# Optimization experiments

Hardware: AMD Instinct MI355X
Metric: run time of the kernel (lower is better)

Reference implementation:

```python
import jax, jax.numpy as jnp
import numpy as np

B, S, D, H = 2, 2048, 1024, 16
HD = D // H  # head dim = 64


def setup_inputs() -> dict:
    key = jax.random.key(0)
    ks = jax.random.split(key, 9)
    sc = 1.0 / np.sqrt(D)
    x = jax.random.normal(ks[0], (B, S, D), dtype=jnp.float32)
    # weights stored as (in, out); y = x @ W + b (same math as torch Linear with W.T)
    Wq = jax.random.normal(ks[1], (D, D), dtype=jnp.float32) * sc
    Wk = jax.random.normal(ks[2], (D, D), dtype=jnp.float32) * sc
    Wv = jax.random.normal(ks[3], (D, D), dtype=jnp.float32) * sc
    Wo = jax.random.normal(ks[4], (D, D), dtype=jnp.float32) * sc
    bq = jax.random.normal(ks[5], (D,), dtype=jnp.float32) * 0.01
    bk = jax.random.normal(ks[6], (D,), dtype=jnp.float32) * 0.01
    bv = jax.random.normal(ks[7], (D,), dtype=jnp.float32) * 0.01
    bo = jax.random.normal(ks[8], (D,), dtype=jnp.float32) * 0.01
    return {"x": x, "Wq": Wq, "bq": bq, "Wk": Wk, "bk": bk,
            "Wv": Wv, "bv": bv, "Wo": Wo, "bo": bo}


def reference(x, Wq, bq, Wk, bk, Wv, bv, Wo, bo):
    b, s, d = x.shape
    q = (x @ Wq + bq).reshape(b, s, H, HD)
    k = (x @ Wk + bk).reshape(b, s, H, HD)
    v = (x @ Wv + bv).reshape(b, s, H, HD)
    # [b, h, s, s] scores, scaled by sqrt(head_dim)
    scores = jnp.einsum('bqhd,bkhd->bhqk', q, k) / np.sqrt(HD)
    causal = jnp.triu(jnp.ones((s, s), dtype=bool), k=1)  # True above diagonal
    scores = jnp.where(causal, -jnp.inf, scores)
    w = jax.nn.softmax(scores, axis=-1)  # dropout rate 0 -> identity
    ctx = jnp.einsum('bhqk,bkhd->bqhd', w, v).reshape(b, s, d)
    return ctx @ Wo + bo
```

## Files before the change

kernel.cpp:

```cpp
#include <hip/hip_runtime.h>
#include <math.h>

#define BB 2
#define SS 2048
#define DD 1024
#define HH 16
#define HDIM 64

typedef __bf16 bf16_t;
typedef __attribute__((ext_vector_type(8))) __bf16 bf16x8;
typedef __attribute__((ext_vector_type(4))) __bf16 bf16x4;
typedef __attribute__((ext_vector_type(4))) float f32x4;

__device__ inline bf16_t f2bf(float f) {
    unsigned int x; __builtin_memcpy(&x, &f, 4);
    unsigned int r = (x + 0x7FFFu + ((x >> 16) & 1u)) >> 16;
    unsigned short us = (unsigned short)r;
    bf16_t b; __builtin_memcpy(&b, &us, 2); return b;
}
__device__ inline unsigned int fbits(float f) {
    unsigned int x; __builtin_memcpy(&x, &f, 4); return x;
}
__device__ inline unsigned int pack_bf2(float a, float b) {
    return ((fbits(a) + 0x8000u) >> 16) | ((fbits(b) + 0x8000u) & 0xFFFF0000u);
}
__device__ inline void gload16(const void* g, void* lds_base) {
    __builtin_amdgcn_global_load_lds(
        (const __attribute__((address_space(1))) void*)g,
        (__attribute__((address_space(3))) void*)lds_base, 16, 0, 0);
}

__global__ __launch_bounds__(256)
void prep_kernel(const float* __restrict__ x, bf16_t* __restrict__ xb,
                 const float* __restrict__ W0, const float* __restrict__ W1,
                 const float* __restrict__ W2, const float* __restrict__ W3,
                 bf16x8* __restrict__ P0, bf16x8* __restrict__ P1,
                 bf16x8* __restrict__ P2, bf16x8* __restrict__ P3) {
    const int y = blockIdx.y;
    const int tid = threadIdx.x;
    if (y == 0) {
        const int i = blockIdx.x * 256 + tid;
        const float4 v = reinterpret_cast<const float4*>(x)[i];
        bf16x4 o;
        o.x = f2bf(v.x); o.y = f2bf(v.y); o.z = f2bf(v.z); o.w = f2bf(v.w);
        reinterpret_cast<bf16x4*>(xb)[i] = o;
    } else {
        if (blockIdx.x >= 512) return;
        const float* W = (y == 1) ? W0 : (y == 2) ? W1 : (y == 3) ? W2 : W3;
        bf16x8* Wp = (y == 1) ? P0 : (y == 2) ? P1 : (y == 3) ? P2 : P3;
        const int t = blockIdx.x * 256 + tid;
        const int g = t >> 10, n = t & 1023;
        bf16x8 v;
        #pragma unroll
        for (int j = 0; j < 8; ++j) v[j] = f2bf(W[(size_t)(g * 8 + j) * DD + n]);
        Wp[(size_t)g * DD + n] = v;
    }
}

template<int MODE>
__global__ __launch_bounds__(256)
void gemm_mfma(const bf16_t* __restrict__ A,
               const bf16x8* __restrict__ Wp0, const bf16x8* __restrict__ Wp1,
               const bf16x8* __restrict__ Wp2,
               const float* __restrict__ b0, const float* __restrict__ b1,
               const float* __restrict__ b2,
               void* __restrict__ C0, void* __restrict__ C1,
               bf16_t* __restrict__ Vt) {
    extern __shared__ char smem[];
    bf16x8 (*As)[8]   = reinterpret_cast<bf16x8(*)[8]>(smem);
    bf16x8 (*Bs)[128] = reinterpret_cast<bf16x8(*)[128]>(smem + 16384);

    const int z = (MODE == 0) ? blockIdx.z : 0;
    const bf16x8* Wp = (z == 0) ? Wp0 : (z == 1) ? Wp1 : Wp2;
    const float* bias = (z == 0) ? b0 : (z == 1) ? b1 : b2;

    const int tid = threadIdx.x;
    const int ln = tid & 63, wv = tid >> 6;
    const int quad = ln >> 4, l15 = ln & 15;
    const int wr = wv >> 1, wc = wv & 1;
    const int m0 = blockIdx.y * 128;
    const int n0 = blockIdx.x * 128;

    int arow[4], acl[4], bg[4], bn[4];
    #pragma unroll
    for (int u = 0; u < 4; ++u) {
        const int S = (wv * 4 + u) * 64 + ln;
        arow[u] = S >> 3; acl[u] = (S & 7) ^ (arow[u] & 7);
        bg[u] = S >> 7;   bn[u] = S & 127;
    }

    f32x4 acc[4][4];
    #pragma unroll
    for (int i = 0; i < 4; ++i)
        #pragma unroll
        for (int j = 0; j < 4; ++j) acc[i][j] = (f32x4){0.f, 0.f, 0.f, 0.f};

    for (int k0 = 0; k0 < DD; k0 += 64) {
        __syncthreads();
        const int kg0 = k0 >> 3;
        #pragma unroll
        for (int u = 0; u < 4; ++u) {
            gload16(&A[(size_t)(m0 + arow[u]) * DD + k0 + acl[u] * 8],
                    smem + (size_t)(wv * 4 + u) * 1024);
            gload16(&Wp[(size_t)(kg0 + bg[u]) * DD + n0 + bn[u]],
                    smem + 16384 + (size_t)(wv * 4 + u) * 1024);
        }
        __syncthreads();

        #pragma unroll
        for (int kk = 0; kk < 2; ++kk) {
            bf16x8 fa[4], fb[4];
            #pragma unroll
            for (int mi = 0; mi < 4; ++mi) {
                const int row = wr * 64 + mi * 16 + l15;
                fa[mi] = As[row][(kk * 4 + quad) ^ (row & 7)];
            }
            #pragma unroll
            for (int ni = 0; ni < 4; ++ni)
                fb[ni] = Bs[kk * 4 + quad][wc * 64 + ni * 16 + l15];
            #pragma unroll
            for (int mi = 0; mi < 4; ++mi)
                #pragma unroll
                for (int ni = 0; ni < 4; ++ni)
                    acc[mi][ni] = __builtin_amdgcn_mfma_f32_16x16x32_bf16(
                        fa[mi], fb[ni], acc[mi][ni], 0, 0, 0);
        }
    }

    if (MODE == 1) {
        float* C = (float*)C0;
        #pragma unroll
        for (int ni = 0; ni < 4; ++ni) {
            const int col = n0 + wc * 64 + ni * 16 + l15;
            const float bv = bias[col];
            #pragma unroll
            for (int mi = 0; mi < 4; ++mi)
                #pragma unroll
                for (int r = 0; r < 4; ++r) {
                    const int row = m0 + wr * 64 + mi * 16 + quad * 4 + r;
                    C[(size_t)row * DD + col] = acc[mi][ni][r] + bv;
                }
        }
    } else if (z < 2) {
        bf16_t* C = (bf16_t*)((z == 0) ? C0 : C1);
        #pragma unroll
        for (int ni = 0; ni < 4; ++ni) {
            const int col = n0 + wc * 64 + ni * 16 + l15;
            const float bv = bias[col];
            #pragma unroll
            for (int mi = 0; mi < 4; ++mi)
                #pragma unroll
                for (int r = 0; r < 4; ++r) {
                    const int row = m0 + wr * 64 + mi * 16 + quad * 4 + r;
                    C[(size_t)row * DD + col] = f2bf(acc[mi][ni][r] + bv);
                }
        }
    } else {
        unsigned short (*T)[136] = reinterpret_cast<unsigned short(*)[136]>(smem);
        __syncthreads();
        #pragma unroll
        for (int ni = 0; ni < 4; ++ni) {
            const int cl = wc * 64 + ni * 16 + l15;
            const float bv = bias[n0 + cl];
            #pragma unroll
            for (int mi = 0; mi < 4; ++mi) {
                const int rl = wr * 64 + mi * 16 + quad * 4;
                uint2 pk;
                pk.x = pack_bf2(acc[mi][ni][0] + bv, acc[mi][ni][1] + bv);
                pk.y = pack_bf2(acc[mi][ni][2] + bv, acc[mi][ni][3] + bv);
                *reinterpret_cast<uint2*>(&T[cl][rl]) = pk;
            }
        }
        __syncthreads();
        const int b = m0 >> 11, s0 = m0 & 2047, h0 = n0 >> 6;
        #pragma unroll
        for (int u = 0; u < 8; ++u) {
            const int c = u * 256 + tid;
            const int s8 = c & 15, nl = c >> 4;
            const bf16x8 v = *reinterpret_cast<const bf16x8*>(&T[nl][s8 * 8]);
            const int bh = b * 16 + h0 + (nl >> 6), d = nl & 63;
            *reinterpret_cast<bf16x8*>(
                &Vt[((size_t)bh * 64 + d) * SS + s0 + s8 * 8]) = v;
        }
    }
}

#define SCL 0.18033688f
#define FM  12.0f

__global__ __launch_bounds__(256)
void attn_mfma(const bf16_t* __restrict__ Q, const bf16_t* __restrict__ Kg,
               const bf16_t* __restrict__ Vt, bf16_t* __restrict__ Ctx) {
    __shared__ bf16x8 Ks[128][8];
    __shared__ bf16x8 Vs[128][8];
    __shared__ unsigned short Ps[4][16][64];

    const int tid = threadIdx.x;
    const int ln = tid & 63, w = tid >> 6;
    const int quad = ln >> 4, l15 = ln & 15;
    const int bh = blockIdx.x;
    const int qt = (blockIdx.y + blockIdx.x) & 31;
    const int b = bh >> 4, h = bh & 15;
    const size_t rowbase = (size_t)b * SS;
    const int col0 = h * 64;

    const int krow0 = w * 16 + (ln >> 3);
    const int krow1 = krow0 + 8;
    const int kc0 = (ln & 7) ^ (krow0 & 7);
    const int kc1 = (ln & 7) ^ (krow1 & 7);

    bf16x8 fq[2];
    {
        const int qrow = qt * 64 + w * 16 + l15;
        #pragma unroll
        for (int kk = 0; kk < 2; ++kk)
            fq[kk] = *reinterpret_cast<const bf16x8*>(
                &Q[(rowbase + qrow) * DD + col0 + kk * 32 + quad * 8]);
    }

    f32x4 acc_o[4];
    #pragma unroll
    for (int i = 0; i < 4; ++i) acc_o[i] = (f32x4){0.f, 0.f, 0.f, 0.f};
    float lsum = 0.f;

    auto stage = [&](int tile, int half) {
        char* kb = (char*)&Ks[half * 64][0] + w * 2048;
        char* vb = (char*)&Vs[half * 64][0] + w * 2048;
        gload16(&Kg[(rowbase + tile * 64 + krow0) * DD + col0 + kc0 * 8], kb);
        gload16(&Kg[(rowbase + tile * 64 + krow1) * DD + col0 + kc1 * 8], kb + 1024);
        gload16(&Vt[((size_t)bh * 64 + krow0) * SS + tile * 64 + kc0 * 8], vb);
        gload16(&Vt[((size_t)bh * 64 + krow1) * SS + tile * 64 + kc1 * 8], vb + 1024);
    };

    unsigned short* const psw = &Ps[w][l15][0];
    const int swz = l15 & 7;

    auto compute_tile = [&](int half, bool diag) {
        const int ro = half * 64;
        #pragma unroll
        for (int ni = 0; ni < 4; ++ni) {
            const int slot = ni * 4 + quad;
            unsigned short* pdst =
                psw + (((slot >> 1) ^ swz) * 8 + (slot & 1) * 4);
            if (diag && ni > w) {
                *reinterpret_cast<uint2*>(pdst) = (uint2){0u, 0u};
                continue;
            }
            f32x4 st = (f32x4){0.f, 0.f, 0.f, 0.f};
            const int krow = ni * 16 + l15;
            #pragma unroll
            for (int kk = 0; kk < 2; ++kk) {
                const bf16x8 fk = Ks[ro + krow][(kk * 4 + quad) ^ (krow & 7)];
                st = __builtin_amdgcn_mfma_f32_16x16x32_bf16(fk, fq[kk], st, 0, 0, 0);
            }
            float p[4];
            #pragma unroll
            for (int r = 0; r < 4; ++r) {
                p[r] = __builtin_amdgcn_exp2f(st[r] * SCL - FM);
                if (diag && ni == w && (quad * 4 + r) > l15) p[r] = 0.f;
            }
            lsum += (p[0] + p[1]) + (p[2] + p[3]);
            uint2 pk;
            pk.x = pack_bf2(p[0], p[1]);
            pk.y = pack_bf2(p[2], p[3]);
            *reinterpret_cast<uint2*>(pdst) = pk;
        }
        #pragma unroll
        for (int kk = 0; kk < 2; ++kk) {
            const bf16x8 fp = *reinterpret_cast<const bf16x8*>(
                psw + ((kk * 4 + quad) ^ swz) * 8);
            #pragma unroll
            for (int nd = 0; nd < 4; ++nd) {
                const int vrow = nd * 16 + l15;
                const bf16x8 fv = Vs[ro + vrow][(kk * 4 + quad) ^ (vrow & 7)];
                acc_o[nd] = __builtin_amdgcn_mfma_f32_16x16x32_bf16(fv, fp, acc_o[nd], 0, 0, 0);
            }
        }
    };

    int kt = 0;
    if ((qt & 1) == 0) {
        stage(0, 0);
        __syncthreads();
        compute_tile(0, qt == 0);
        kt = 1;
    }
    for (; kt < qt; kt += 2) {
        __syncthreads();
        stage(kt, 0);
        stage(kt + 1, 1);
        __syncthreads();
        compute_tile(0, false);
        compute_tile(1, kt + 1 == qt);
    }

    lsum += __shfl_xor(lsum, 16);
    lsum += __shfl_xor(lsum, 32);
    const float inv = 1.f / lsum;

    const size_t orow = (rowbase + qt * 64 + w * 16 + l15) * DD + col0;
    #pragma unroll
    for (int nd = 0; nd < 4; ++nd) {
        uint2 ov;
        ov.x = pack_bf2(acc_o[nd][0] * inv, acc_o[nd][1] * inv);
        ov.y = pack_bf2(acc_o[nd][2] * inv, acc_o[nd][3] * inv);
        *reinterpret_cast<uint2*>(&Ctx[orow + nd * 16 + quad * 4]) = ov;
    }
}

extern "C" void kernel_launch(void* const* d_in, const int* in_sizes, int n_in,
                              void* d_out, int out_size, void* d_ws, size_t ws_size,
                              hipStream_t stream) {
    const float* x  = (const float*)d_in[0];
    const float* Wq = (const float*)d_in[1];
    const float* bq = (const float*)d_in[2];
    const float* Wk = (const float*)d_in[3];
    const float* bk = (const float*)d_in[4];
    const float* Wv = (const float*)d_in[5];
    const float* bv = (const float*)d_in[6];
    const float* Wo = (const float*)d_in[7];
    const float* bo = (const float*)d_in[8];
    float* out = (float*)d_out;

    const size_t M = (size_t)BB * SS;
    const size_t mat = M * DD;
    const size_t wsz = (size_t)DD * DD;

    bf16_t* ws = (bf16_t*)d_ws;
    bf16_t* xb   = ws;
    bf16_t* Wqp  = ws + mat;
    bf16_t* Wkp  = Wqp + wsz;
    bf16_t* Wvp  = Wkp + wsz;
    bf16_t* Wop  = Wvp + wsz;
    bf16_t* Qb   = Wop + wsz;
    bf16_t* Kb   = Qb + mat;
    bf16_t* Vtb  = Kb + mat;
    bf16_t* Ctxb = Vtb + mat;

    dim3 blk(256);
    hipLaunchKernelGGL(prep_kernel, dim3(4096, 5), blk, 0, stream,
                       x, xb, Wq, Wk, Wv, Wo,
                       (bf16x8*)Wqp, (bf16x8*)Wkp, (bf16x8*)Wvp, (bf16x8*)Wop);

    hipLaunchKernelGGL((gemm_mfma<0>), dim3(DD / 128, M / 128, 3), blk, 34816, stream,
                       xb, (const bf16x8*)Wqp, (const bf16x8*)Wkp, (const bf16x8*)Wvp,
                       bq, bk, bv, Qb, Kb, Vtb);

    hipLaunchKernelGGL(attn_mfma, dim3(BB * HH, SS / 64), blk, 0, stream,
                       Qb, Kb, Vtb, Ctxb);

    hipLaunchKernelGGL((gemm_mfma<1>), dim3(DD / 128, M / 128, 1), blk, 32768, stream,
                       Ctxb, (const bf16x8*)Wop, (const bf16x8*)Wop, (const bf16x8*)Wop,
                       bo, bo, bo, out, out, nullptr);
}
```

Measured before the change: 199.3 us.

## Enlarge attention query tile, add narrow output GEMM, compact prep grid

Attention now processes 128 query rows per block, two 16-row groups per wave, so each staged K/V tile is reused for twice as many queries, halving K/V loads per query. Query tiles are paired so blocks with short and long causal ranges interleave. The output projection moves to a dedicated kernel with 128x64 tiles, doubling block count for better CU occupancy. The prep kernel drops idle blocks and processes all four weights per thread. More registers per attention wave may reduce occupancy.

```diff
diff --git a/kernel.cpp b/kernel.cpp
--- a/kernel.cpp
+++ b/kernel.cpp
@@ -36,41 +36,45 @@
                  const float* __restrict__ W2, const float* __restrict__ W3,
                  bf16x8* __restrict__ P0, bf16x8* __restrict__ P1,
                  bf16x8* __restrict__ P2, bf16x8* __restrict__ P3) {
-    const int y = blockIdx.y;
-    const int tid = threadIdx.x;
-    if (y == 0) {
-        const int i = blockIdx.x * 256 + tid;
-        const float4 v = reinterpret_cast<const float4*>(x)[i];
-        bf16x4 o;
-        o.x = f2bf(v.x); o.y = f2bf(v.y); o.z = f2bf(v.z); o.w = f2bf(v.w);
-        reinterpret_cast<bf16x4*>(xb)[i] = o;
+    const int bid = blockIdx.x, tid = threadIdx.x;
+    if (bid < 2048) {
+        const int i = bid * 512 + tid;
+        #pragma unroll
+        for (int u = 0; u < 2; ++u) {
+            const int j = i + u * 256;
+            const float4 v = reinterpret_cast<const float4*>(x)[j];
+            bf16x4 o;
+            o.x = f2bf(v.x); o.y = f2bf(v.y); o.z = f2bf(v.z); o.w = f2bf(v.w);
+            reinterpret_cast<bf16x4*>(xb)[j] = o;
+        }
     } else {
-        if (blockIdx.x >= 512) return;
-        const float* W = (y == 1) ? W0 : (y == 2) ? W1 : (y == 3) ? W2 : W3;
-        bf16x8* Wp = (y == 1) ? P0 : (y == 2) ? P1 : (y == 3) ? P2 : P3;
-        const int t = blockIdx.x * 256 + tid;
+        const int t = (bid - 2048) * 256 + tid;
         const int g = t >> 10, n = t & 1023;
-        bf16x8 v;
-        #pragma unroll
-        for (int j = 0; j < 8; ++j) v[j] = f2bf(W[(size_t)(g * 8 + j) * DD + n]);
-        Wp[(size_t)g * DD + n] = v;
-    }
-}
-
-template<int MODE>
+        const float* Ws[4] = {W0, W1, W2, W3};
+        bf16x8* Pp[4] = {P0, P1, P2, P3};
+        #pragma unroll
+        for (int m = 0; m < 4; ++m) {
+            bf16x8 v;
+            #pragma unroll
+            for (int j = 0; j < 8; ++j) v[j] = f2bf(Ws[m][(size_t)(g * 8 + j) * DD + n]);
+            Pp[m][(size_t)g * DD + n] = v;
+        }
+    }
+}
+
 __global__ __launch_bounds__(256)
-void gemm_mfma(const bf16_t* __restrict__ A,
-               const bf16x8* __restrict__ Wp0, const bf16x8* __restrict__ Wp1,
-               const bf16x8* __restrict__ Wp2,
-               const float* __restrict__ b0, const float* __restrict__ b1,
-               const float* __restrict__ b2,
-               void* __restrict__ C0, void* __restrict__ C1,
-               bf16_t* __restrict__ Vt) {
+void gemm_qkv(const bf16_t* __restrict__ A,
+              const bf16x8* __restrict__ Wp0, const bf16x8* __restrict__ Wp1,
+              const bf16x8* __restrict__ Wp2,
+              const float* __restrict__ b0, const float* __restrict__ b1,
+              const float* __restrict__ b2,
+              bf16_t* __restrict__ C0, bf16_t* __restrict__ C1,
+              bf16_t* __restrict__ Vt) {
     extern __shared__ char smem[];
     bf16x8 (*As)[8]   = reinterpret_cast<bf16x8(*)[8]>(smem);
     bf16x8 (*Bs)[128] = reinterpret_cast<bf16x8(*)[128]>(smem + 16384);
 
-    const int z = (MODE == 0) ? blockIdx.z : 0;
+    const int z = blockIdx.z;
     const bf16x8* Wp = (z == 0) ? Wp0 : (z == 1) ? Wp1 : Wp2;
     const float* bias = (z == 0) ? b0 : (z == 1) ? b1 : b2;
 
@@ -127,22 +131,8 @@
         }
     }
 
-    if (MODE == 1) {
-        float* C = (float*)C0;
-        #pragma unroll
-        for (int ni = 0; ni < 4; ++ni) {
-            const int col = n0 + wc * 64 + ni * 16 + l15;
-            const float bv = bias[col];
-            #pragma unroll
-            for (int mi = 0; mi < 4; ++mi)
-                #pragma unroll
-                for (int r = 0; r < 4; ++r) {
-                    const int row = m0 + wr * 64 + mi * 16 + quad * 4 + r;
-                    C[(size_t)row * DD + col] = acc[mi][ni][r] + bv;
-                }
-        }
-    } else if (z < 2) {
-        bf16_t* C = (bf16_t*)((z == 0) ? C0 : C1);
+    if (z < 2) {
+        bf16_t* C = (z == 0) ? C0 : C1;
         #pragma unroll
         for (int ni = 0; ni < 4; ++ni) {
             const int col = n0 + wc * 64 + ni * 16 + l15;
@@ -185,6 +175,84 @@
     }
 }
 
+__global__ __launch_bounds__(256)
+void gemm_out(const bf16_t* __restrict__ A, const bf16x8* __restrict__ Wp,
+              const float* __restrict__ bias, float* __restrict__ C) {
+    __shared__ bf16x8 As[128][8];
+    __shared__ bf16x8 Bs[8][64];
+
+    const int tid = threadIdx.x;
+    const int ln = tid & 63, wv = tid >> 6;
+    const int quad = ln >> 4, l15 = ln & 15;
+    const int wr = wv >> 1, wc = wv & 1;
+    const int m0 = blockIdx.y * 128;
+    const int n0 = blockIdx.x * 64;
+
+    int arow[4], acl[4], bkg[2], bn[2];
+    #pragma unroll
+    for (int u = 0; u < 4; ++u) {
+        const int S = (wv * 4 + u) * 64 + ln;
+        arow[u] = S >> 3; acl[u] = (S & 7) ^ (arow[u] & 7);
+    }
+    #pragma unroll
+    for (int u = 0; u < 2; ++u) {
+        const int S = (wv * 2 + u) * 64 + ln;
+        bkg[u] = S >> 6; bn[u] = S & 63;
+    }
+
+    f32x4 acc[4][2];
+    #pragma unroll
+    for (int i = 0; i < 4; ++i)
+        #pragma unroll
+        for (int j = 0; j < 2; ++j) acc[i][j] = (f32x4){0.f, 0.f, 0.f, 0.f};
+
+    for (int k0 = 0; k0 < DD; k0 += 64) {
+        __syncthreads();
+        const int kg0 = k0 >> 3;
+        #pragma unroll
+        for (int u = 0; u < 4; ++u)
+            gload16(&A[(size_t)(m0 + arow[u]) * DD + k0 + acl[u] * 8],
+                    (char*)&As[0][0] + (size_t)(wv * 4 + u) * 1024);
+        #pragma unroll
+        for (int u = 0; u < 2; ++u)
+            gload16(&Wp[(size_t)(kg0 + bkg[u]) * DD + n0 + bn[u]],
+                    (char*)&Bs[0][0] + (size_t)(wv * 2 + u) * 1024);
+        __syncthreads();
+
+        #pragma unroll
+        for (int kk = 0; kk < 2; ++kk) {
+            bf16x8 fa[4], fb[2];
+            #pragma unroll
+            for (int mi = 0; mi < 4; ++mi) {
+                const int row = wr * 64 + mi * 16 + l15;
+                fa[mi] = As[row][(kk * 4 + quad) ^ (row & 7)];
+            }
+            #pragma unroll
+            for (int ni = 0; ni < 2; ++ni)
+                fb[ni] = Bs[kk * 4 + quad][wc * 32 + ni * 16 + l15];
+            #pragma unroll
+            for (int mi = 0; mi < 4; ++mi)
+                #pragma unroll
+                for (int ni = 0; ni < 2; ++ni)
+                    acc[mi][ni] = __builtin_amdgcn_mfma_f32_16x16x32_bf16(
+                        fa[mi], fb[ni], acc[mi][ni], 0, 0, 0);
+        }
+    }
+
+    #pragma unroll
+    for (int ni = 0; ni < 2; ++ni) {
+        const int col = n0 + wc * 32 + ni * 16 + l15;
+        const float bv = bias[col];
+        #pragma unroll
+        for (int mi = 0; mi < 4; ++mi)
+            #pragma unroll
+            for (int r = 0; r < 4; ++r) {
+                const int row = m0 + wr * 64 + mi * 16 + quad * 4 + r;
+                C[(size_t)row * DD + col] = acc[mi][ni][r] + bv;
+            }
+    }
+}
+
 #define SCL 0.18033688f
 #define FM  12.0f
 
@@ -193,13 +261,14 @@
                const bf16_t* __restrict__ Vt, bf16_t* __restrict__ Ctx) {
     __shared__ bf16x8 Ks[128][8];
     __shared__ bf16x8 Vs[128][8];
-    __shared__ unsigned short Ps[4][16][64];
+    __shared__ unsigned short Ps[4][2][16][64];
 
     const int tid = threadIdx.x;
     const int ln = tid & 63, w = tid >> 6;
     const int quad = ln >> 4, l15 = ln & 15;
     const int bh = blockIdx.x;
-    const int qt = (blockIdx.y + blockIdx.x) & 31;
+    const int tswz = (blockIdx.x + blockIdx.y) & 7;
+    const int qt = (blockIdx.y < 8) ? tswz : 15 - tswz;
     const int b = bh >> 4, h = bh & 15;
     const size_t rowbase = (size_t)b * SS;
     const int col0 = h * 64;
@@ -209,19 +278,22 @@
     const int kc0 = (ln & 7) ^ (krow0 & 7);
     const int kc1 = (ln & 7) ^ (krow1 & 7);
 
-    bf16x8 fq[2];
-    {
-        const int qrow = qt * 64 + w * 16 + l15;
+    bf16x8 fq[2][2];
+    #pragma unroll
+    for (int rg = 0; rg < 2; ++rg) {
+        const int qrow = qt * 128 + w * 32 + rg * 16 + l15;
         #pragma unroll
         for (int kk = 0; kk < 2; ++kk)
-            fq[kk] = *reinterpret_cast<const bf16x8*>(
+            fq[rg][kk] = *reinterpret_cast<const bf16x8*>(
                 &Q[(rowbase + qrow) * DD + col0 + kk * 32 + quad * 8]);
     }
 
-    f32x4 acc_o[4];
-    #pragma unroll
-    for (int i = 0; i < 4; ++i) acc_o[i] = (f32x4){0.f, 0.f, 0.f, 0.f};
-    float lsum = 0.f;
+    f32x4 acc_o[2][4];
+    #pragma unroll
+    for (int rg = 0; rg < 2; ++rg)
+        #pragma unroll
+        for (int i = 0; i < 4; ++i) acc_o[rg][i] = (f32x4){0.f, 0.f, 0.f, 0.f};
+    float lsum[2] = {0.f, 0.f};
 
     auto stage = [&](int tile, int half) {
         char* kb = (char*)&Ks[half * 64][0] + w * 2048;
@@ -232,79 +304,94 @@
         gload16(&Vt[((size_t)bh * 64 + krow1) * SS + tile * 64 + kc1 * 8], vb + 1024);
     };
 
-    unsigned short* const psw = &Ps[w][l15][0];
     const int swz = l15 & 7;
 
-    auto compute_tile = [&](int half, bool diag) {
-        const int ro = half * 64;
-        #pragma unroll
-        for (int ni = 0; ni < 4; ++ni) {
-            const int slot = ni * 4 + quad;
-            unsigned short* pdst =
-                psw + (((slot >> 1) ^ swz) * 8 + (slot & 1) * 4);
-            if (diag && ni > w) {
-                *reinterpret_cast<uint2*>(pdst) = (uint2){0u, 0u};
-                continue;
-            }
-            f32x4 st = (f32x4){0.f, 0.f, 0.f, 0.f};
-            const int krow = ni * 16 + l15;
-            #pragma unroll
-            for (int kk = 0; kk < 2; ++kk) {
-                const bf16x8 fk = Ks[ro + krow][(kk * 4 + quad) ^ (krow & 7)];
-                st = __builtin_amdgcn_mfma_f32_16x16x32_bf16(fk, fq[kk], st, 0, 0, 0);
-            }
-            float p[4];
-            #pragma unroll
-            for (int r = 0; r < 4; ++r) {
-                p[r] = __builtin_amdgcn_exp2f(st[r] * SCL - FM);
-                if (diag && ni == w && (quad * 4 + r) > l15) p[r] = 0.f;
-            }
-            lsum += (p[0] + p[1]) + (p[2] + p[3]);
-            uint2 pk;
-            pk.x = pack_bf2(p[0], p[1]);
-            pk.y = pack_bf2(p[2], p[3]);
-            *reinterpret_cast<uint2*>(pdst) = pk;
+    auto compute_tile = [&](int ro, int dq0, int dq1) {
+        const int dq[2] = {dq0, dq1};
+        #pragma unroll
+        for (int rg = 0; rg < 2; ++rg) {
+            if (dq[rg] < 0) continue;
+            unsigned short* const psw = &Ps[w][rg][l15][0];
+            #pragma unroll
+            for (int ni = 0; ni < 4; ++ni) {
+                const int slot = ni * 4 + quad;
+                unsigned short* pdst = psw + (((slot >> 1) ^ swz) * 8 + (slot & 1) * 4);
+                const int g = ni * 16;
+                if (g > dq[rg]) {
+                    *reinterpret_cast<uint2*>(pdst) = (uint2){0u, 0u};
+                    continue;
+                }
+                f32x4 st = (f32x4){0.f, 0.f, 0.f, 0.f};
+                const int krow = ni * 16 + l15;
+                #pragma unroll
+                for (int kk = 0; kk < 2; ++kk) {
+                    const bf16x8 fk = Ks[ro + krow][(kk * 4 + quad) ^ (krow & 7)];
+                    st = __builtin_amdgcn_mfma_f32_16x16x32_bf16(fk, fq[rg][kk], st, 0, 0, 0);
+                }
+                float p[4];
+                #pragma unroll
+                for (int r = 0; r < 4; ++r) {
+                    p[r] = __builtin_amdgcn_exp2f(st[r] * SCL - FM);
+                    if (g == dq[rg] && (quad * 4 + r) > l15) p[r] = 0.f;
+                }
+                lsum[rg] += (p[0] + p[1]) + (p[2] + p[3]);
+                uint2 pk;
+                pk.x = pack_bf2(p[0], p[1]);
+                pk.y = pack_bf2(p[2], p[3]);
+                *reinterpret_cast<uint2*>(pdst) = pk;
+            }
         }
         #pragma unroll
         for (int kk = 0; kk < 2; ++kk) {
-            const bf16x8 fp = *reinterpret_cast<const bf16x8*>(
-                psw + ((kk * 4 + quad) ^ swz) * 8);
+            bf16x8 fp[2];
+            #pragma unroll
+            for (int rg = 0; rg < 2; ++rg)
+                fp[rg] = *reinterpret_cast<const bf16x8*>(
+                    &Ps[w][rg][l15][(((kk * 4 + quad) ^ swz) * 8)]);
             #pragma unroll
             for (int nd = 0; nd < 4; ++nd) {
                 const int vrow = nd * 16 + l15;
                 const bf16x8 fv = Vs[ro + vrow][(kk * 4 + quad) ^ (vrow & 7)];
-                acc_o[nd] = __builtin_amdgcn_mfma_f32_16x16x32_bf16(fv, fp, acc_o[nd], 0, 0, 0);
+                if (dq0 >= 0)
+                    acc_o[0][nd] = __builtin_amdgcn_mfma_f32_16x16x32_bf16(fv, fp[0], acc_o[0][nd], 0, 0, 0);
+                if (dq1 >= 0)
+                    acc_o[1][nd] = __builtin_amdgcn_mfma_f32_16x16x32_bf16(fv, fp[1], acc_o[1][nd], 0, 0, 0);
             }
         }
     };
 
-    int kt = 0;
-    if ((qt & 1) == 0) {
-        stage(0, 0);
-        __syncthreads();
-        compute_tile(0, qt == 0);
-        kt = 1;
-    }
-    for (; kt < qt; kt += 2) {
-        __syncthreads();
-        stage(kt, 0);
-        stage(kt + 1, 1);
-        __syncthreads();
-        compute_tile(0, false);
-        compute_tile(1, kt + 1 == qt);
-    }
-
-    lsum += __shfl_xor(lsum, 16);
-    lsum += __shfl_xor(lsum, 32);
-    const float inv = 1.f / lsum;
-
-    const size_t orow = (rowbase + qt * 64 + w * 16 + l15) * DD + col0;
-    #pragma unroll
-    for (int nd = 0; nd < 4; ++nd) {
-        uint2 ov;
-        ov.x = pack_bf2(acc_o[nd][0] * inv, acc_o[nd][1] * inv);
-        ov.y = pack_bf2(acc_o[nd][2] * inv, acc_o[nd][3] * inv);
-        *reinterpret_cast<uint2*>(&Ctx[orow + nd * 16 + quad * 4]) = ov;
+    for (int p = 0; p < qt; ++p) {
+        __syncthreads();
+        stage(2 * p, 0);
+        stage(2 * p + 1, 1);
+        __syncthreads();
+        compute_tile(0, 112, 112);
+        compute_tile(64, 112, 112);
+    }
+    {
+        __syncthreads();
+        stage(2 * qt, 0);
+        stage(2 * qt + 1, 1);
+        __syncthreads();
+        const int lq0 = w * 32, lq1 = w * 32 + 16;
+        compute_tile(0, lq0, lq1);
+        compute_tile(64, lq0 - 64, lq1 - 64);
+    }
+
+    #pragma unroll
+    for (int rg = 0; rg < 2; ++rg) {
+        float s = lsum[rg];
+        s += __shfl_xor(s, 16);
+        s += __shfl_xor(s, 32);
+        const float inv = 1.f / s;
+        const size_t orow = (rowbase + qt * 128 + w * 32 + rg * 16 + l15) * DD + col0;
+        #pragma unroll
+        for (int nd = 0; nd < 4; ++nd) {
+            uint2 ov;
+            ov.x = pack_bf2(acc_o[rg][nd][0] * inv, acc_o[rg][nd][1] * inv);
+            ov.y = pack_bf2(acc_o[rg][nd][2] * inv, acc_o[rg][nd][3] * inv);
+            *reinterpret_cast<uint2*>(&Ctx[orow + nd * 16 + quad * 4]) = ov;
+        }
     }
 }
 
@@ -338,18 +425,17 @@
     bf16_t* Ctxb = Vtb + mat;
 
     dim3 blk(256);
-    hipLaunchKernelGGL(prep_kernel, dim3(4096, 5), blk, 0, stream,
+    hipLaunchKernelGGL(prep_kernel, dim3(2560), blk, 0, stream,
                        x, xb, Wq, Wk, Wv, Wo,
                        (bf16x8*)Wqp, (bf16x8*)Wkp, (bf16x8*)Wvp, (bf16x8*)Wop);
 
-    hipLaunchKernelGGL((gemm_mfma<0>), dim3(DD / 128, M / 128, 3), blk, 34816, stream,
+    hipLaunchKernelGGL(gemm_qkv, dim3(DD / 128, M / 128, 3), blk, 34816, stream,
                        xb, (const bf16x8*)Wqp, (const bf16x8*)Wkp, (const bf16x8*)Wvp,
                        bq, bk, bv, Qb, Kb, Vtb);
 
-    hipLaunchKernelGGL(attn_mfma, dim3(BB * HH, SS / 64), blk, 0, stream,
+    hipLaunchKernelGGL(attn_mfma, dim3(BB * HH, SS / 128), blk, 0, stream,
                        Qb, Kb, Vtb, Ctxb);
 
-    hipLaunchKernelGGL((gemm_mfma<1>), dim3(DD / 128, M / 128, 1), blk, 32768, stream,
-                       Ctxb, (const bf16x8*)Wop, (const bf16x8*)Wop, (const bf16x8*)Wop,
-                       bo, bo, bo, out, out, nullptr);
-}
+    hipLaunchKernelGGL(gemm_out, dim3(DD / 64, M / 128), blk, 0, stream,
+                       Ctxb, (const bf16x8*)Wop, bo, out);
+}
```

After: 196.1 us. Within noise of the previous version (-1.6%).
